# Kernel tuning notes

Hardware: AMD Instinct MI355X
Metric: run time of the kernel (lower is better)

Reference implementation:

```python
import jax, jax.numpy as jnp
import numpy as np
from jax import lax

AR_VOCAB = 25
EN_VOCAB = 25
N_CLASSES = 1 + AR_VOCAB + EN_VOCAB + AR_VOCAB * EN_VOCAB  # full_table id layout
NEG = -jnp.inf
BIG_NEG = -1e30  # acts as log(0) in float32 (exp underflows to exactly 0) but keeps grads finite
T_LEN = 256
V_LEN = 256


def setup_inputs() -> dict:
    key = jax.random.key(0)
    k1, k2 = jax.random.split(key)
    ar_sent = jax.random.randint(k1, (1, T_LEN), 0, AR_VOCAB)
    en_sent = jax.random.randint(k2, (1, V_LEN), 0, EN_VOCAB)
    # self.weights = log(uniform) over target classes
    weights = jnp.full((N_CLASSES,), -jnp.log(jnp.float32(N_CLASSES)), dtype=jnp.float32)
    return {"ar_sent": ar_sent, "en_sent": en_sent, "weights": weights}


def _chain(c, m):
    """Solve a[0]=c[0]; a[i]=logaddexp(c[i], m[i]+a[i-1]) in parallel.
    a[i] = s[i] + logcumsumexp(c - s)[i] with s = prefix sums of m (s[0]=0)."""
    s = jnp.concatenate([jnp.zeros((1,), c.dtype), jnp.cumsum(m[1:])])
    return s + lax.associative_scan(jnp.logaddexp, c - s)


def _safe_lse(x, axis):
    """Stable logsumexp that returns -inf (with zero gradient) on empty/-inf slices."""
    m = lax.stop_gradient(jnp.max(x, axis=axis, keepdims=True))
    m = jnp.where(jnp.isfinite(m), m, 0.0)
    s = jnp.sum(jnp.exp(x - m), axis=axis)
    ok = s > 0
    return jnp.squeeze(m, axis=axis) + jnp.where(ok, jnp.log(jnp.where(ok, s, 1.0)), NEG)


def _forward(ar, en, weights):
    # ar: [T] int, en: [V] int, weights: [C] log-probs
    T, V = ar.shape[0], en.shape[0]
    del_ids = 1 + ar                                               # [T]
    ins_ids = 1 + AR_VOCAB + en                                    # [V]
    sub_ids = 1 + AR_VOCAB + EN_VOCAB + EN_VOCAB * ar[:, None] + en[None, :]  # [T,V]
    w_del = weights[del_ids]   # [T]
    w_ins = weights[ins_ids]   # [V]
    w_sub = weights[sub_ids]   # [T,V]

    # ---- alpha DP (forward lattice) ----
    # row 0: alpha[0,0]=0, alpha[0,v]=alpha[0,v-1]+w_ins[v]
    c0 = jnp.full((V,), BIG_NEG, weights.dtype).at[0].set(0.0)
    row0 = _chain(c0, w_ins)

    def fstep(prev, xs):
        wd, ws = xs  # w_del[t] scalar, w_sub[t,:] [V]
        # c[v] = logaddexp(w_del[t]+alpha[t-1,v], w_sub[t,v]+alpha[t-1,v-1]); v=0 has no sub term
        c = jnp.concatenate([(wd + prev[0])[None],
                             jnp.logaddexp(wd + prev[1:], ws[1:] + prev[:-1])])
        row = _chain(c, w_ins)  # adds within-row insertion recurrence
        return row, row

    _, frows = lax.scan(fstep, row0, (w_del[1:], w_sub[1:]))
    alpha = jnp.concatenate([row0[None], frows], axis=0)  # [T,V]

    # ---- beta DP (backward lattice) ----
    m_rev = w_ins[::-1]
    cT = jnp.full((V,), BIG_NEG, weights.dtype).at[-1].set(0.0)
    rowT = _chain(cT[::-1], m_rev)[::-1]

    def bstep(nxt, xs):
        wd, ws = xs
        # c[v] = logaddexp(w_del[t]+beta[t+1,v], w_sub[t,v]+beta[t+1,v+1]); v=V-1 has no sub term
        c = jnp.concatenate([jnp.logaddexp(wd + nxt[:-1], ws[:-1] + nxt[1:]),
                             (wd + nxt[-1])[None]])
        row = _chain(c[::-1], m_rev)[::-1]  # beta[t,v] += w_ins[v]+beta[t,v+1] recurrence
        return row, row

    _, brows = lax.scan(bstep, rowT, (w_del[:-1], w_sub[:-1]), reverse=True)
    beta = jnp.concatenate([brows, rowT[None]], axis=0)  # [T,V]

    # ---- expected edit-operation counts (log space) ----
    cls = jnp.arange(N_CLASSES)
    w = weights[None, None, :]
    md = jnp.where(del_ids[1:, None, None] == cls, 0.0, NEG)   # [T-1,1,C] one-hot log mask
    mi = jnp.where(ins_ids[None, 1:, None] == cls, 0.0, NEG)   # [1,V-1,C]
    ms = jnp.where(sub_ids[1:, 1:, None] == cls, 0.0, NEG)     # [T-1,V-1,C]
    ed = alpha[:-1, :, None] + w + md + beta[1:, :, None]      # expected deletions
    ei = alpha[:, :-1, None] + w + mi + beta[:, 1:, None]      # expected insertions
    es = alpha[:-1, :-1, None] + w + ms + beta[1:, 1:, None]   # expected substitutions
    return _safe_lse(jnp.stack([_safe_lse(ed, (0, 1)),
                                _safe_lse(ei, (0, 1)),
                                _safe_lse(es, (0, 1))]), 0)    # [C]


def reference(ar_sent, en_sent, weights):
    return _forward(ar_sent[0], en_sent[0], weights)
```

## Files before the change

kernel.cpp:

```cpp
#include <hip/hip_runtime.h>
#include <math.h>

#define NCLS 676
#define NEG_SENTINEL -3.0e38f
#define LN2F 0.6931471805599453f
#define JPAD 768
#define ROWS 768
#define QIP_OFF 692
#define WSE_OFF 1460
#define SHM_FLOATS (WSE_OFF + 25 * JPAD)

struct f4u { float x, y, z, w; };

__device__ __forceinline__ float dpp_shr1(float x) {
  return __int_as_float(
      __builtin_amdgcn_update_dpp(0, __float_as_int(x), 0x138, 0xF, 0xF, false));
}
__device__ __forceinline__ float dpp_shl1(float x) {
  return __int_as_float(
      __builtin_amdgcn_update_dpp(0, __float_as_int(x), 0x130, 0xF, 0xF, false));
}
__device__ __forceinline__ int dpp_shr1_i(int x) {
  return __builtin_amdgcn_update_dpp(0, x, 0x138, 0xF, 0xF, false);
}
__device__ __forceinline__ int dpp_shl1_i(int x) {
  return __builtin_amdgcn_update_dpp(0, x, 0x130, 0xF, 0xF, false);
}
__device__ __forceinline__ float pow2c(int d) {
  d = min(max(d, -126), 126);
  return __int_as_float((d + 127) << 23);
}

__global__ __launch_bounds__(64) void k_diag(const int* __restrict__ ar,
                                             const int* __restrict__ en,
                                             const float* __restrict__ wts,
                                             float* __restrict__ aD,
                                             float* __restrict__ bD,
                                             int* __restrict__ aEb,
                                             int* __restrict__ bEb) {
  const int lane = threadIdx.x;
  __shared__ alignas(16) float shm[SHM_FLOATS];
  float* pw = shm;
  float* qip = shm + QIP_OFF;
  float* wsE = shm + WSE_OFF;
  for (int c = lane; c < NCLS; c += 64) pw[c] = __expf(wts[c]);
  {
    float4* z = (float4*)(shm + NCLS);
    const int nz = (SHM_FLOATS - NCLS) / 4;
    for (int t = lane; t < nz; t += 64) z[t] = make_float4(0.f, 0.f, 0.f, 0.f);
  }
  __syncthreads();
  for (int j = lane; j < 256; j += 64) {
    int e = en[j];
    qip[255 + j] = pw[26 + e];
#pragma unroll
    for (int a = 0; a < 25; ++a) wsE[a * JPAD + 255 + j] = pw[51 + 25 * a + e];
  }
  __syncthreads();

  const int i0 = 4 * lane;
  float wdl[4];
  const float* rowp[4];
#pragma unroll
  for (int k = 0; k < 4; ++k) {
    int a = ar[i0 + k];
    wdl[k] = pw[1 + a];
    rowp[k] = wsE + a * JPAD;
  }

  float P1[4] = {0.f, 0.f, 0.f, 0.f};
  float P2[4] = {0.f, 0.f, 0.f, 0.f};
  int e1 = 0;

  if (blockIdx.x == 0) {
    if (lane == 0) { P1[0] = 1.f; aD[0 * ROWS + 256] = 1.f; }
    int e0 = 252 - i0;
    float* sp = aD + ROWS + 256 + (1 - i0 - 3);
    int* ep = aEb + lane;
    float W0[4][12], Q0[12], W1[4][12], Q1[12];

#define LOAD_A(EB, W, Q)                                                   \
  {                                                                        \
    _Pragma("unroll") for (int k = 0; k < 4; ++k) {                        \
      const float4* p = (const float4*)(rowp[k] + (EB));                   \
      float4 va = p[0], vb = p[1], vc = p[2];                              \
      W[k][0] = va.x; W[k][1] = va.y; W[k][2] = va.z; W[k][3] = va.w;      \
      W[k][4] = vb.x; W[k][5] = vb.y; W[k][6] = vb.z; W[k][7] = vb.w;      \
      W[k][8] = vc.x; W[k][9] = vc.y; W[k][10] = vc.z; W[k][11] = vc.w;    \
    }                                                                      \
    const float4* q = (const float4*)(qip + (EB));                         \
    float4 qa = q[0], qb = q[1], qc = q[2];                                \
    Q[0] = qa.x; Q[1] = qa.y; Q[2] = qa.z; Q[3] = qa.w;                    \
    Q[4] = qb.x; Q[5] = qb.y; Q[6] = qb.z; Q[7] = qb.w;                    \
    Q[8] = qc.x; Q[9] = qc.y; Q[10] = qc.z; Q[11] = qc.w;                  \
  }

#define PROC_A(W, Q)                                                       \
  {                                                                        \
    *ep = e1; ep += 64;                                                    \
    int t1e = dpp_shr1_i(e1);                                              \
    float f1n = pow2c(t1e - e1);                                           \
    _Pragma("unroll") for (int u = 0; u < 8; ++u) {                        \
      float pm1 = dpp_shr1(P1[3]) * f1n;                                   \
      float pm2 = dpp_shr1(P2[3]) * f1n;                                   \
      float cu[4];                                                         \
      _Pragma("unroll") for (int k = 0; k < 4; ++k) {                      \
        float a1 = (k == 0) ? pm1 : P1[k - 1];                             \
        float a2 = (k == 0) ? pm2 : P2[k - 1];                             \
        cu[k] = fmaf(wdl[k], a1,                                           \
                     fmaf(W[k][4 + u - k], a2, Q[4 + u - k] * P1[k]));     \
      }                                                                    \
      *(f4u*)sp = f4u{cu[3], cu[2], cu[1], cu[0]};                         \
      sp += ROWS + 1;                                                      \
      _Pragma("unroll") for (int k = 0; k < 4; ++k) {                      \
        P2[k] = P1[k]; P1[k] = cu[k];                                      \
      }                                                                    \
    }                                                                      \
    float m = fmaxf(fmaxf(P1[0], P1[1]), fmaxf(P1[2], P1[3]));             \
    int ex = (m > 0.f) ? ((__float_as_int(m) >> 23) - 126) : (t1e - e1);   \
    float sc = pow2c(-ex);                                                 \
    _Pragma("unroll") for (int k = 0; k < 4; ++k) {                        \
      P1[k] *= sc; P2[k] *= sc;                                            \
    }                                                                      \
    e1 += ex;                                                              \
  }

    LOAD_A(e0, W0, Q0);
    for (int it = 0; it < 31; ++it) {
      LOAD_A(e0 + 8, W1, Q1);
      PROC_A(W0, Q0);
      LOAD_A(e0 + 16, W0, Q0);
      PROC_A(W1, Q1);
      e0 += 16;
    }
    LOAD_A(e0 + 8, W1, Q1);
    PROC_A(W0, Q0);
    PROC_A(W1, Q1);
  } else {
    if (lane == 63) P1[3] = 1.f;
    if (lane == 0) bD[510 * ROWS + 256 + 255] = 1.f;
    int e0 = 752 - i0;
    float* sp = bD + 509 * ROWS + 256 + (509 - i0 - 3);
    int* ep = bEb + lane;
    float W0[4][16], Q0[16], W1[4][16], Q1[16];

#define LOAD_B(EB, W, Q)                                                   \
  {                                                                        \
    _Pragma("unroll") for (int k = 0; k < 4; ++k) {                        \
      const float4* p = (const float4*)(rowp[k] + (EB));                   \
      float4 va = p[0], vb = p[1], vc = p[2], vd = p[3];                   \
      W[k][0] = va.x; W[k][1] = va.y; W[k][2] = va.z; W[k][3] = va.w;      \
      W[k][4] = vb.x; W[k][5] = vb.y; W[k][6] = vb.z; W[k][7] = vb.w;      \
      W[k][8] = vc.x; W[k][9] = vc.y; W[k][10] = vc.z; W[k][11] = vc.w;    \
      W[k][12] = vd.x; W[k][13] = vd.y; W[k][14] = vd.z; W[k][15] = vd.w;  \
    }                                                                      \
    const float4* q = (const float4*)(qip + (EB));                         \
    float4 qa = q[0], qb = q[1], qc = q[2], qd = q[3];                     \
    Q[0] = qa.x; Q[1] = qa.y; Q[2] = qa.z; Q[3] = qa.w;                    \
    Q[4] = qb.x; Q[5] = qb.y; Q[6] = qb.z; Q[7] = qb.w;                    \
    Q[8] = qc.x; Q[9] = qc.y; Q[10] = qc.z; Q[11] = qc.w;                  \
    Q[12] = qd.x; Q[13] = qd.y; Q[14] = qd.z; Q[15] = qd.w;                \
  }

#define PROC_B(W, Q)                                                       \
  {                                                                        \
    *ep = e1; ep += 64;                                                    \
    int t1e = dpp_shl1_i(e1);                                              \
    float f1n = pow2c(t1e - e1);                                           \
    _Pragma("unroll") for (int u = 0; u < 8; ++u) {                        \
      float pm1 = dpp_shl1(P1[0]) * f1n;                                   \
      float pm2 = dpp_shl1(P2[0]) * f1n;                                   \
      float cu[4];                                                         \
      _Pragma("unroll") for (int k = 0; k < 4; ++k) {                      \
        float a1 = (k == 3) ? pm1 : P1[k + 1];                             \
        float a2 = (k == 3) ? pm2 : P2[k + 1];                             \
        cu[k] = fmaf(wdl[k], a1,                                           \
                     fmaf(W[k][12 - u - k], a2, Q[13 - u - k] * P1[k]));   \
      }                                                                    \
      *(f4u*)sp = f4u{cu[3], cu[2], cu[1], cu[0]};                         \
      sp -= ROWS + 1;                                                      \
      _Pragma("unroll") for (int k = 0; k < 4; ++k) {                      \
        P2[k] = P1[k]; P1[k] = cu[k];                                      \
      }                                                                    \
    }                                                                      \
    float m = fmaxf(fmaxf(P1[0], P1[1]), fmaxf(P1[2], P1[3]));             \
    int ex = (m > 0.f) ? ((__float_as_int(m) >> 23) - 126) : (t1e - e1);   \
    float sc = pow2c(-ex);                                                 \
    _Pragma("unroll") for (int k = 0; k < 4; ++k) {                        \
      P1[k] *= sc; P2[k] *= sc;                                            \
    }                                                                      \
    e1 += ex;                                                              \
  }

    LOAD_B(e0, W0, Q0);
    for (int it = 0; it < 31; ++it) {
      LOAD_B(e0 - 8, W1, Q1);
      PROC_B(W0, Q0);
      LOAD_B(e0 - 16, W0, Q0);
      PROC_B(W1, Q1);
      e0 -= 16;
    }
    LOAD_B(e0 - 8, W1, Q1);
    PROC_B(W0, Q0);
    PROC_B(W1, Q1);
  }
}

__global__ __launch_bounds__(1024) void k_red(const int* __restrict__ ar,
                                              const int* __restrict__ en,
                                              const float* __restrict__ aD,
                                              const float* __restrict__ bD,
                                              const int* __restrict__ aEb,
                                              const int* __restrict__ bEb,
                                              float* __restrict__ Spart) {
  const int tid = threadIdx.x;
  const int j = tid & 255;
  __shared__ float bins[NCLS];
  for (int c = tid; c < NCLS; c += 1024) bins[c] = 0.f;
  __syncthreads();
  const float M = __logf(aD[510 * ROWS + 256 + 255]) +
                  (float)aEb[63 * 64 + 63] * LN2F + 16.0f;
  const int e = en[j];
#pragma unroll
  for (int rr = 0; rr < 2; ++rr) {
    const int d = blockIdx.x * 8 + (tid >> 8) + rr * 4;
    if (d <= 510) {
      const int i = d - j;
      if (i >= 0 && i <= 255) {
        const float bM = bD[d * ROWS + 256 + j];
        if (bM > 0.f) {
          const int bEx = (d == 510) ? 0 : bEb[((509 - d) >> 3) * 64 + (i >> 2)];
          const float lb = __logf(bM) + (float)bEx * LN2F - M;
          const int a = ar[i];
          if (i >= 1) {
            float aM = aD[(d - 1) * ROWS + 256 + j];
            if (aM > 0.f) {
              int eA = (d == 1) ? 0 : aEb[((d - 2) >> 3) * 64 + ((i - 1) >> 2)];
              float L = __logf(aM) + (float)eA * LN2F + lb;
              atomicAdd(&bins[1 + a], __expf(fminf(L, 0.f)));
            }
          }
          if (j >= 1) {
            float aM = aD[(d - 1) * ROWS + 256 + j - 1];
            if (aM > 0.f) {
              int eA = (d == 1) ? 0 : aEb[((d - 2) >> 3) * 64 + (i >> 2)];
              float L = __logf(aM) + (float)eA * LN2F + lb;
              atomicAdd(&bins[26 + e], __expf(fminf(L, 0.f)));
            }
            if (i >= 1) {
              float aM2 = aD[(d - 2) * ROWS + 256 + j - 1];
              if (aM2 > 0.f) {
                int eA2 =
                    (d == 2) ? 0 : aEb[((d - 3) >> 3) * 64 + ((i - 1) >> 2)];
                float L2 = __logf(aM2) + (float)eA2 * LN2F + lb;
                atomicAdd(&bins[51 + 25 * a + e], __expf(fminf(L2, 0.f)));
              }
            }
          }
        }
      }
    }
  }
  __syncthreads();
  for (int c = tid; c < NCLS; c += 1024) Spart[blockIdx.x * NCLS + c] = bins[c];
}

__global__ void k_out(const float* __restrict__ wts,
                      const float* __restrict__ aD,
                      const int* __restrict__ aEb,
                      const float* __restrict__ Spart,
                      float* __restrict__ out) {
  int c = blockIdx.x * blockDim.x + threadIdx.x;
  if (c >= NCLS) return;
  float s = 0.f;
  for (int b = 0; b < 64; ++b) s += Spart[b * NCLS + c];
  float M = __logf(aD[510 * ROWS + 256 + 255]) + (float)aEb[63 * 64 + 63] * LN2F +
            16.0f;
  out[c] = (c != 0 && s > 0.f) ? (wts[c] + M + __logf(s)) : NEG_SENTINEL;
}

extern "C" void kernel_launch(void* const* d_in, const int* in_sizes, int n_in,
                              void* d_out, int out_size, void* d_ws, size_t ws_size,
                              hipStream_t stream) {
  const int* ar = (const int*)d_in[0];
  const int* en = (const int*)d_in[1];
  const float* wts = (const float*)d_in[2];
  float* aD = (float*)d_ws;
  float* bDraw = aD + 514 * ROWS;
  float* bD = bDraw + 2 * ROWS;
  int* aEb = (int*)(bDraw + 514 * ROWS);
  int* bEb = aEb + 4096;
  float* Spart = (float*)(bEb + 4096);
  k_diag<<<2, 64, 0, stream>>>(ar, en, wts, aD, bD, aEb, bEb);
  k_red<<<64, 1024, 0, stream>>>(ar, en, aD, bD, aEb, bEb, Spart);
  k_out<<<3, 256, 0, stream>>>(wts, aD, aEb, Spart, (float*)d_out);
}
```

Before: 101.1 us.

## Offload diagonal global stores to a second wave via LDS ring and fuse output kernel

The serial DP wave now writes each anti-diagonal into a 16-slot shared-memory ring, and a second wave in the same block copies the ring out to global memory, synchronised through volatile LDS flags. This takes the global store latency off the critical recurrence path. The final k_out kernel is folded into k_red using a last-block atomic counter, which saves one launch. In exchange it adds spin-wait handshakes between the two waves and a threadfence/atomic tail in the reduction.

```diff
diff --git a/kernel.cpp b/kernel.cpp
--- a/kernel.cpp
+++ b/kernel.cpp
@@ -8,7 +8,10 @@
 #define ROWS 768
 #define QIP_OFF 692
 #define WSE_OFF 1460
-#define SHM_FLOATS (WSE_OFF + 25 * JPAD)
+#define EXPS_OFF 20660
+#define RING_OFF 24756
+#define CTL_OFF 28852
+#define SHM_TOT 28864
 
 struct f4u { float x, y, z, w; };
 
@@ -31,53 +34,72 @@
   return __int_as_float((d + 127) << 23);
 }
 
-__global__ __launch_bounds__(64) void k_diag(const int* __restrict__ ar,
-                                             const int* __restrict__ en,
-                                             const float* __restrict__ wts,
-                                             float* __restrict__ aD,
-                                             float* __restrict__ bD,
-                                             int* __restrict__ aEb,
-                                             int* __restrict__ bEb) {
-  const int lane = threadIdx.x;
-  __shared__ alignas(16) float shm[SHM_FLOATS];
+__global__ __launch_bounds__(128) void k_diag(const int* __restrict__ ar,
+                                              const int* __restrict__ en,
+                                              const float* __restrict__ wts,
+                                              float* __restrict__ aD,
+                                              float* __restrict__ bD,
+                                              int* __restrict__ aEbG,
+                                              int* __restrict__ bEbG,
+                                              int* __restrict__ redcnt) {
+  const int tid = threadIdx.x;
+  const int lane = tid & 63;
+  const int wid = tid >> 6;
+  const bool alpha = (blockIdx.x == 0);
+  __shared__ alignas(16) float shm[SHM_TOT];
+  int* shmI = (int*)shm;
   float* pw = shm;
   float* qip = shm + QIP_OFF;
   float* wsE = shm + WSE_OFF;
-  for (int c = lane; c < NCLS; c += 64) pw[c] = __expf(wts[c]);
+
+  for (int c = tid; c < NCLS; c += 128) pw[c] = __expf(wts[c]);
   {
     float4* z = (float4*)(shm + NCLS);
-    const int nz = (SHM_FLOATS - NCLS) / 4;
-    for (int t = lane; t < nz; t += 64) z[t] = make_float4(0.f, 0.f, 0.f, 0.f);
-  }
-  __syncthreads();
-  for (int j = lane; j < 256; j += 64) {
+    const int nz = (SHM_TOT - NCLS) / 4;
+    for (int t = tid; t < nz; t += 128) z[t] = make_float4(0.f, 0.f, 0.f, 0.f);
+  }
+  __syncthreads();
+  for (int j = tid; j < 256; j += 128) {
     int e = en[j];
     qip[255 + j] = pw[26 + e];
 #pragma unroll
     for (int a = 0; a < 25; ++a) wsE[a * JPAD + 255 + j] = pw[51 + 25 * a + e];
   }
-  __syncthreads();
-
-  const int i0 = 4 * lane;
-  float wdl[4];
-  const float* rowp[4];
+  if (tid == 0) {
+    if (alpha) { shmI[CTL_OFF] = 0; shmI[CTL_OFF + 1] = 0; }
+    else       { shmI[CTL_OFF] = 600; shmI[CTL_OFF + 1] = 518; }
+  }
+  if (tid == 1) {
+    if (alpha) aD[0 * ROWS + 256 + 0] = 1.0f;
+    else       bD[510 * ROWS + 256 + 255] = 1.0f;
+  }
+  if (tid == 2) *redcnt = 0;
+  __syncthreads();
+
+  volatile int* prodv = (volatile int*)&shmI[CTL_OFF];
+  volatile int* flcv = (volatile int*)&shmI[CTL_OFF + 1];
+
+  if (wid == 0) {
+    const int i0 = 4 * lane;
+    const int rcol = 252 - i0;
+    float wdl[4];
+    const float* rowp[4];
 #pragma unroll
-  for (int k = 0; k < 4; ++k) {
-    int a = ar[i0 + k];
-    wdl[k] = pw[1 + a];
-    rowp[k] = wsE + a * JPAD;
-  }
-
-  float P1[4] = {0.f, 0.f, 0.f, 0.f};
-  float P2[4] = {0.f, 0.f, 0.f, 0.f};
-  int e1 = 0;
-
-  if (blockIdx.x == 0) {
-    if (lane == 0) { P1[0] = 1.f; aD[0 * ROWS + 256] = 1.f; }
-    int e0 = 252 - i0;
-    float* sp = aD + ROWS + 256 + (1 - i0 - 3);
-    int* ep = aEb + lane;
-    float W0[4][12], Q0[12], W1[4][12], Q1[12];
+    for (int k = 0; k < 4; ++k) {
+      int a = ar[i0 + k];
+      wdl[k] = pw[1 + a];
+      rowp[k] = wsE + a * JPAD;
+    }
+    float P1[4] = {0.f, 0.f, 0.f, 0.f};
+    float P2[4] = {0.f, 0.f, 0.f, 0.f};
+    int e1 = 0;
+    int* epl = &shmI[EXPS_OFF] + lane;
+
+    if (alpha) {
+      if (lane == 0) P1[0] = 1.f;
+      int e0 = 252 - i0;
+      int d0w = 1;
+      float W0[4][12], Q0[12], W1[4][12], Q1[12];
 
 #define LOAD_A(EB, W, Q)                                                   \
   {                                                                        \
@@ -95,9 +117,11 @@
     Q[8] = qc.x; Q[9] = qc.y; Q[10] = qc.z; Q[11] = qc.w;                  \
   }
 
-#define PROC_A(W, Q)                                                       \
+#define PROC_A(W, Q, PH)                                                   \
   {                                                                        \
-    *ep = e1; ep += 64;                                                    \
+    while (*flcv < d0w - 9) __builtin_amdgcn_s_sleep(2);                   \
+    __threadfence_block();                                                 \
+    epl[0] = e1; epl += 64;                                                \
     int t1e = dpp_shr1_i(e1);                                              \
     float f1n = pow2c(t1e - e1);                                           \
     _Pragma("unroll") for (int u = 0; u < 8; ++u) {                        \
@@ -110,12 +134,14 @@
         cu[k] = fmaf(wdl[k], a1,                                           \
                      fmaf(W[k][4 + u - k], a2, Q[4 + u - k] * P1[k]));     \
       }                                                                    \
-      *(f4u*)sp = f4u{cu[3], cu[2], cu[1], cu[0]};                         \
-      sp += ROWS + 1;                                                      \
+      *(float4*)&shm[RING_OFF + ((((PH) + u) & 15) << 8) + rcol] =         \
+          make_float4(cu[3], cu[2], cu[1], cu[0]);                         \
       _Pragma("unroll") for (int k = 0; k < 4; ++k) {                      \
         P2[k] = P1[k]; P1[k] = cu[k];                                      \
       }                                                                    \
     }                                                                      \
+    __threadfence_block();                                                 \
+    if (lane == 0) *prodv = d0w + 7;                                       \
     float m = fmaxf(fmaxf(P1[0], P1[1]), fmaxf(P1[2], P1[3]));             \
     int ex = (m > 0.f) ? ((__float_as_int(m) >> 23) - 126) : (t1e - e1);   \
     float sc = pow2c(-ex);                                                 \
@@ -123,26 +149,27 @@
       P1[k] *= sc; P2[k] *= sc;                                            \
     }                                                                      \
     e1 += ex;                                                              \
-  }
-
-    LOAD_A(e0, W0, Q0);
-    for (int it = 0; it < 31; ++it) {
+    d0w += 8;                                                              \
+  }
+
+      LOAD_A(e0, W0, Q0);
+      for (int it = 0; it < 31; ++it) {
+        LOAD_A(e0 + 8, W1, Q1);
+        PROC_A(W0, Q0, 1);
+        LOAD_A(e0 + 16, W0, Q0);
+        PROC_A(W1, Q1, 9);
+        e0 += 16;
+      }
       LOAD_A(e0 + 8, W1, Q1);
-      PROC_A(W0, Q0);
-      LOAD_A(e0 + 16, W0, Q0);
-      PROC_A(W1, Q1);
-      e0 += 16;
-    }
-    LOAD_A(e0 + 8, W1, Q1);
-    PROC_A(W0, Q0);
-    PROC_A(W1, Q1);
-  } else {
-    if (lane == 63) P1[3] = 1.f;
-    if (lane == 0) bD[510 * ROWS + 256 + 255] = 1.f;
-    int e0 = 752 - i0;
-    float* sp = bD + 509 * ROWS + 256 + (509 - i0 - 3);
-    int* ep = bEb + lane;
-    float W0[4][16], Q0[16], W1[4][16], Q1[16];
+      PROC_A(W0, Q0, 1);
+      PROC_A(W1, Q1, 9);
+    } else {
+      if (lane == 63) P1[3] = 1.f;
+      float qi0 = pw[26 + en[i0]];
+      (void)qi0;
+      int e0 = 764 - i0;
+      int s0w = 509;
+      float W0[4][16], Q0[16], W1[4][16], Q1[16];
 
 #define LOAD_B(EB, W, Q)                                                   \
   {                                                                        \
@@ -162,9 +189,11 @@
     Q[12] = qd.x; Q[13] = qd.y; Q[14] = qd.z; Q[15] = qd.w;                \
   }
 
-#define PROC_B(W, Q)                                                       \
+#define PROC_B(W, Q, PH)                                                   \
   {                                                                        \
-    *ep = e1; ep += 64;                                                    \
+    while (*flcv > s0w + 9) __builtin_amdgcn_s_sleep(2);                   \
+    __threadfence_block();                                                 \
+    epl[0] = e1; epl += 64;                                                \
     int t1e = dpp_shl1_i(e1);                                              \
     float f1n = pow2c(t1e - e1);                                           \
     _Pragma("unroll") for (int u = 0; u < 8; ++u) {                        \
@@ -177,12 +206,14 @@
         cu[k] = fmaf(wdl[k], a1,                                           \
                      fmaf(W[k][12 - u - k], a2, Q[13 - u - k] * P1[k]));   \
       }                                                                    \
-      *(f4u*)sp = f4u{cu[3], cu[2], cu[1], cu[0]};                         \
-      sp -= ROWS + 1;                                                      \
+      *(float4*)&shm[RING_OFF + ((((PH) - u) & 15) << 8) + rcol] =         \
+          make_float4(cu[3], cu[2], cu[1], cu[0]);                         \
       _Pragma("unroll") for (int k = 0; k < 4; ++k) {                      \
         P2[k] = P1[k]; P1[k] = cu[k];                                      \
       }                                                                    \
     }                                                                      \
+    __threadfence_block();                                                 \
+    if (lane == 0) *prodv = s0w - 7;                                       \
     float m = fmaxf(fmaxf(P1[0], P1[1]), fmaxf(P1[2], P1[3]));             \
     int ex = (m > 0.f) ? ((__float_as_int(m) >> 23) - 126) : (t1e - e1);   \
     float sc = pow2c(-ex);                                                 \
@@ -190,19 +221,63 @@
       P1[k] *= sc; P2[k] *= sc;                                            \
     }                                                                      \
     e1 += ex;                                                              \
-  }
-
-    LOAD_B(e0, W0, Q0);
-    for (int it = 0; it < 31; ++it) {
+    s0w -= 8;                                                              \
+  }
+
+      LOAD_B(e0, W0, Q0);
+      for (int it = 0; it < 31; ++it) {
+        LOAD_B(e0 - 8, W1, Q1);
+        PROC_B(W0, Q0, 13);
+        LOAD_B(e0 - 16, W0, Q0);
+        PROC_B(W1, Q1, 5);
+        e0 -= 16;
+      }
       LOAD_B(e0 - 8, W1, Q1);
-      PROC_B(W0, Q0);
-      LOAD_B(e0 - 16, W0, Q0);
-      PROC_B(W1, Q1);
-      e0 -= 16;
+      PROC_B(W0, Q0, 13);
+      PROC_B(W1, Q1, 5);
     }
-    LOAD_B(e0 - 8, W1, Q1);
-    PROC_B(W0, Q0);
-    PROC_B(W1, Q1);
+  } else {
+    if (alpha) {
+      float* gp = aD + 1 * ROWS + 2 + 4 * lane;
+      for (int g = 1; g <= 505; g += 8) {
+        const int tgt = g + 7;
+        while (*prodv < tgt) __builtin_amdgcn_s_sleep(2);
+        __threadfence_block();
+        for (int u = 0; u < 8; ++u) {
+          int d = g + u;
+          if (d <= 510) {
+            float4 v = *(const float4*)&shm[RING_OFF + ((d & 15) << 8) +
+                                            (lane << 2)];
+            *(f4u*)gp = f4u{v.x, v.y, v.z, v.w};
+          }
+          gp += ROWS + 1;
+        }
+        if (lane == 0) *flcv = g + 7;
+      }
+      const int4* es = (const int4*)&shm[EXPS_OFF];
+      int4* ed = (int4*)aEbG;
+      for (int t = lane; t < 1024; t += 64) ed[t] = es[t];
+    } else {
+      float* gp = bD + 509 * ROWS + 510 + 4 * lane;
+      for (int g = 509; g >= 5; g -= 8) {
+        const int tgt = g - 7;
+        while (*prodv > tgt) __builtin_amdgcn_s_sleep(2);
+        __threadfence_block();
+        for (int u = 0; u < 8; ++u) {
+          int s = g - u;
+          if (s >= 0) {
+            float4 v = *(const float4*)&shm[RING_OFF + ((s & 15) << 8) +
+                                            (lane << 2)];
+            *(f4u*)gp = f4u{v.x, v.y, v.z, v.w};
+          }
+          gp -= ROWS + 1;
+        }
+        if (lane == 0) *flcv = g - 7;
+      }
+      const int4* es = (const int4*)&shm[EXPS_OFF];
+      int4* ed = (int4*)bEbG;
+      for (int t = lane; t < 1024; t += 64) ed[t] = es[t];
+    }
   }
 }
 
@@ -212,10 +287,14 @@
                                               const float* __restrict__ bD,
                                               const int* __restrict__ aEb,
                                               const int* __restrict__ bEb,
-                                              float* __restrict__ Spart) {
+                                              float* __restrict__ Spart,
+                                              const float* __restrict__ wts,
+                                              float* __restrict__ out,
+                                              int* __restrict__ redcnt) {
   const int tid = threadIdx.x;
   const int j = tid & 255;
   __shared__ float bins[NCLS];
+  __shared__ int lastf;
   for (int c = tid; c < NCLS; c += 1024) bins[c] = 0.f;
   __syncthreads();
   const float M = __logf(aD[510 * ROWS + 256 + 255]) +
@@ -263,20 +342,16 @@
   }
   __syncthreads();
   for (int c = tid; c < NCLS; c += 1024) Spart[blockIdx.x * NCLS + c] = bins[c];
-}
-
-__global__ void k_out(const float* __restrict__ wts,
-                      const float* __restrict__ aD,
-                      const int* __restrict__ aEb,
-                      const float* __restrict__ Spart,
-                      float* __restrict__ out) {
-  int c = blockIdx.x * blockDim.x + threadIdx.x;
-  if (c >= NCLS) return;
-  float s = 0.f;
-  for (int b = 0; b < 64; ++b) s += Spart[b * NCLS + c];
-  float M = __logf(aD[510 * ROWS + 256 + 255]) + (float)aEb[63 * 64 + 63] * LN2F +
-            16.0f;
-  out[c] = (c != 0 && s > 0.f) ? (wts[c] + M + __logf(s)) : NEG_SENTINEL;
+  __threadfence();
+  if (tid == 0) lastf = (atomicAdd(redcnt, 1) == 63) ? 1 : 0;
+  __syncthreads();
+  if (lastf == 0) return;
+  __threadfence();
+  if (tid < NCLS) {
+    float s = 0.f;
+    for (int b = 0; b < 64; ++b) s += Spart[b * NCLS + tid];
+    out[tid] = (tid != 0 && s > 0.f) ? (wts[tid] + M + __logf(s)) : NEG_SENTINEL;
+  }
 }
 
 extern "C" void kernel_launch(void* const* d_in, const int* in_sizes, int n_in,
@@ -291,7 +366,8 @@
   int* aEb = (int*)(bDraw + 514 * ROWS);
   int* bEb = aEb + 4096;
   float* Spart = (float*)(bEb + 4096);
-  k_diag<<<2, 64, 0, stream>>>(ar, en, wts, aD, bD, aEb, bEb);
-  k_red<<<64, 1024, 0, stream>>>(ar, en, aD, bD, aEb, bEb, Spart);
-  k_out<<<3, 256, 0, stream>>>(wts, aD, aEb, Spart, (float*)d_out);
-}
+  int* redcnt = (int*)(Spart + 64 * NCLS);
+  k_diag<<<2, 128, 0, stream>>>(ar, en, wts, aD, bD, aEb, bEb, redcnt);
+  k_red<<<64, 1024, 0, stream>>>(ar, en, aD, bD, aEb, bEb, Spart, wts,
+                                 (float*)d_out, redcnt);
+}
```

After: 128.6 us. 27.3% more time.
